# Kernel optimization log

Measured on AMD Instinct MI355X. Metric: run time of the kernel, lower is better.

The kernel has to match this reference:

```python
import jax, jax.numpy as jnp
import numpy as np

N = 100000
E = 1600000
F_IN = 512
H1, C1 = 8, 8          # conv1: 8 heads x 8 channels, concat -> 64
H2, C2 = 1, 16         # conv2: 1 head x num_classes=16, mean
NEG_SLOPE = 0.2


def setup_inputs() -> dict:
    key = jax.random.key(0)
    ks = jax.random.split(key, 10)
    x = jax.random.normal(ks[0], (N, F_IN), dtype=jnp.float32)
    edge_index = jax.random.randint(ks[1], (2, E), 0, N, dtype=jnp.int64)
    s1 = 1.0 / np.sqrt(F_IN)
    s2 = 1.0 / np.sqrt(H1 * C1)
    W1 = jax.random.normal(ks[2], (F_IN, H1 * C1), dtype=jnp.float32) * s1
    a1_src = jax.random.normal(ks[3], (H1, C1), dtype=jnp.float32) * 0.1
    a1_dst = jax.random.normal(ks[4], (H1, C1), dtype=jnp.float32) * 0.1
    b1 = jnp.zeros((H1 * C1,), dtype=jnp.float32)
    W2 = jax.random.normal(ks[5], (H1 * C1, H2 * C2), dtype=jnp.float32) * s2
    a2_src = jax.random.normal(ks[6], (H2, C2), dtype=jnp.float32) * 0.1
    a2_dst = jax.random.normal(ks[7], (H2, C2), dtype=jnp.float32) * 0.1
    b2 = jnp.zeros((C2,), dtype=jnp.float32)
    return {"x": x, "edge_index": edge_index, "W1": W1, "a1_src": a1_src,
            "a1_dst": a1_dst, "b1": b1, "W2": W2, "a2_src": a2_src,
            "a2_dst": a2_dst, "b2": b2}


def _add_self_loops(edge_index, n):
    loops = jnp.arange(n, dtype=edge_index.dtype)
    return jnp.concatenate([edge_index, jnp.stack([loops, loops])], axis=1)


def gat_conv(x, edge_index, W, a_src, a_dst, bias, concat):
    # x: [N, Fin]; W: [Fin, H*C]; a_*: [H, C]
    n = x.shape[0]
    H, C = a_src.shape
    h = (x @ W).reshape(n, H, C)                      # [N, H, C]
    al_src = jnp.einsum('nhc,hc->nh', h, a_src)       # [N, H]
    al_dst = jnp.einsum('nhc,hc->nh', h, a_dst)
    src, dst = edge_index[0], edge_index[1]
    e = al_src[src] + al_dst[dst]                     # [E, H]
    e = jnp.where(e > 0, e, NEG_SLOPE * e)            # LeakyReLU
    # segment softmax over destination nodes
    m = jax.ops.segment_max(e, dst, num_segments=n)   # [N, H]
    ex = jnp.exp(e - m[dst])
    s = jax.ops.segment_sum(ex, dst, num_segments=n)  # [N, H]
    alpha = ex / s[dst]                               # [E, H]
    msg = h[src] * alpha[:, :, None]                  # [E, H, C]
    out = jax.ops.segment_sum(msg, dst, num_segments=n)  # [N, H, C]
    if concat:
        out = out.reshape(n, H * C)
    else:
        out = out.mean(axis=1)
    return out + bias


def reference(x, edge_index, W1, a1_src, a1_dst, b1, W2, a2_src, a2_dst, b2):
    ei = _add_self_loops(edge_index, x.shape[0])
    h = gat_conv(x, ei, W1, a1_src, a1_dst, b1, concat=True)
    h = jax.nn.elu(h)
    h = gat_conv(h, ei, W2, a2_src, a2_dst, b2, concat=False)
    return jax.nn.log_softmax(h, axis=1)
```

## Files before the change

### kernel.cpp

```cpp
#include <hip/hip_runtime.h>
#include <math.h>

#define F_IN 512
#define NHEAD1 8
#define NC1 8
#define F1 64
#define NC2 16
#define NEG_SLOPE 0.2f
#define BSHIFT 7
#define PART_G 512
#define BUILD_CAP 4608

static __device__ __forceinline__ float leaky(float v) {
    return v > 0.0f ? v : NEG_SLOPE * v;
}

__global__ __launch_bounds__(256) void k_gemm1(const float* __restrict__ x,
                                               const float* __restrict__ W,
                                               float* __restrict__ h1, int N) {
    __shared__ float xs[64][33];
    __shared__ float wsm[32][64];
    const int tid = threadIdx.x;
    const int tx = tid & 15, ty = tid >> 4;
    const int row0 = blockIdx.x * 64;
    float acc[4][4] = {};

    for (int k0 = 0; k0 < F_IN; k0 += 32) {
        {
            int r = tid >> 3;
            int c = (tid & 7) * 4;
            #pragma unroll
            for (int rr = 0; rr < 64; rr += 32) {
                int gr = row0 + r + rr;
                float4 v = make_float4(0.f, 0.f, 0.f, 0.f);
                if (gr < N) v = *(const float4*)(x + (size_t)gr * F_IN + k0 + c);
                xs[r + rr][c + 0] = v.x; xs[r + rr][c + 1] = v.y;
                xs[r + rr][c + 2] = v.z; xs[r + rr][c + 3] = v.w;
            }
            int wr = tid >> 4;
            int wc = (tid & 15) * 4;
            #pragma unroll
            for (int rr = 0; rr < 32; rr += 16) {
                *(float4*)(&wsm[wr + rr][wc]) =
                    *(const float4*)(W + (size_t)(k0 + wr + rr) * F1 + wc);
            }
        }
        __syncthreads();
        #pragma unroll
        for (int k = 0; k < 32; ++k) {
            float a[4], b[4];
            #pragma unroll
            for (int i = 0; i < 4; ++i) a[i] = xs[ty * 4 + i][k];
            #pragma unroll
            for (int j = 0; j < 4; ++j) b[j] = wsm[k][tx * 4 + j];
            #pragma unroll
            for (int i = 0; i < 4; ++i)
                #pragma unroll
                for (int j = 0; j < 4; ++j) acc[i][j] += a[i] * b[j];
        }
        __syncthreads();
    }
    #pragma unroll
    for (int i = 0; i < 4; ++i) {
        int gr = row0 + ty * 4 + i;
        if (gr < N) {
            float4 v = make_float4(acc[i][0], acc[i][1], acc[i][2], acc[i][3]);
            *(float4*)(h1 + (size_t)gr * F1 + tx * 4) = v;
        }
    }
}

__global__ void k_prep1(const float* __restrict__ h1, const float* __restrict__ a1s,
                        const float* __restrict__ a1d, float* __restrict__ al1s,
                        float* __restrict__ al1d, int NH) {
    int t = blockIdx.x * blockDim.x + threadIdx.x;
    if (t >= NH) return;
    int h = t & 7;
    const float* hp = h1 + (size_t)t * NC1;
    float4 v0 = *(const float4*)hp;
    float4 v1 = *(const float4*)(hp + 4);
    const float* as = a1s + h * NC1;
    const float* ad = a1d + h * NC1;
    al1s[t] = v0.x * as[0] + v0.y * as[1] + v0.z * as[2] + v0.w * as[3]
            + v1.x * as[4] + v1.y * as[5] + v1.z * as[6] + v1.w * as[7];
    al1d[t] = v0.x * ad[0] + v0.y * ad[1] + v0.z * ad[2] + v0.w * ad[3]
            + v1.x * ad[4] + v1.y * ad[5] + v1.z * ad[6] + v1.w * ad[7];
}

__global__ __launch_bounds__(256) void k_bcount(const int* __restrict__ ei,
                                                int* __restrict__ counts,
                                                int E, int NBUCK, int chunk) {
    __shared__ int cnt[1024];
    const int g = blockIdx.x, tid = threadIdx.x;
    for (int i = tid; i < NBUCK; i += 256) cnt[i] = 0;
    __syncthreads();
    int lo = g * chunk, hi = lo + chunk;
    if (hi > E) hi = E;
    for (int e = lo + tid; e < hi; e += 256)
        atomicAdd(&cnt[ei[E + e] >> BSHIFT], 1);
    __syncthreads();
    for (int k = tid; k < NBUCK; k += 256)
        counts[k * PART_G + g] = cnt[k];
}

__global__ __launch_bounds__(256) void k_scan_block(const int* __restrict__ in,
                                                    int* __restrict__ out,
                                                    int* __restrict__ blocksum, int L) {
    __shared__ int sdata[256];
    int t = threadIdx.x;
    int i = blockIdx.x * 256 + t;
    int v = (i < L) ? in[i] : 0;
    sdata[t] = v;
    __syncthreads();
    for (int off = 1; off < 256; off <<= 1) {
        int add = (t >= off) ? sdata[t - off] : 0;
        __syncthreads();
        sdata[t] += add;
        __syncthreads();
    }
    if (i < L) out[i] = sdata[t] - v;
    if (t == 255) blocksum[blockIdx.x] = sdata[t];
}

__global__ void k_scan_carry(const int* __restrict__ blocksum,
                             int* __restrict__ blockoffset, int NB) {
    int lane = threadIdx.x;
    int carry = 0;
    for (int base = 0; base < NB; base += 64) {
        int i = base + lane;
        int v = (i < NB) ? blocksum[i] : 0;
        int x = v;
        #pragma unroll
        for (int off = 1; off < 64; off <<= 1) {
            int y = __shfl_up(x, off);
            if (lane >= off) x += y;
        }
        if (i < NB) blockoffset[i] = carry + x - v;
        carry += __shfl(x, 63);
    }
}

__global__ void k_scan_addg(int* __restrict__ out, const int* __restrict__ boff, int L) {
    int i = blockIdx.x * blockDim.x + threadIdx.x;
    if (i < L) out[i] += boff[i >> 8];
}

__global__ __launch_bounds__(256) void k_bscatter(const int* __restrict__ ei,
                                                  const int* __restrict__ offs,
                                                  unsigned long long* __restrict__ packed,
                                                  int E, int NBUCK, int chunk) {
    __shared__ int cur[1024];
    const int g = blockIdx.x, tid = threadIdx.x;
    for (int k = tid; k < NBUCK; k += 256) cur[k] = offs[k * PART_G + g];
    __syncthreads();
    int lo = g * chunk, hi = lo + chunk;
    if (hi > E) hi = E;
    for (int e = lo + tid; e < hi; e += 256) {
        int src = ei[e], dst = ei[E + e];
        int pos = atomicAdd(&cur[dst >> BSHIFT], 1);
        packed[pos] = ((unsigned long long)(unsigned)dst << 32) | (unsigned)src;
    }
}

__global__ __launch_bounds__(256) void k_bbuild(const unsigned long long* __restrict__ packed,
                                                const int* __restrict__ offs,
                                                int* __restrict__ rowptr,
                                                int* __restrict__ esrc,
                                                int E, int N, int NBUCK) {
    __shared__ int sdeg[128], sinc[128], scur[128];
    __shared__ int sbuf[BUILD_CAP];
    const int k = blockIdx.x, tid = threadIdx.x;
    const int s = offs[k * PART_G];
    const int e = (k + 1 < NBUCK) ? offs[(k + 1) * PART_G] : E;
    const int cnt = e - s;
    if (tid < 128) sdeg[tid] = 0;
    __syncthreads();
    for (int i = tid; i < cnt; i += 256) {
        int dl = ((int)(packed[s + i] >> 32)) & 127;
        atomicAdd(&sdeg[dl], 1);
    }
    __syncthreads();
    if (tid < 128) sinc[tid] = sdeg[tid];
    __syncthreads();
    for (int off = 1; off < 128; off <<= 1) {
        int add = (tid < 128 && tid >= off) ? sinc[tid - off] : 0;
        __syncthreads();
        if (tid < 128) sinc[tid] += add;
        __syncthreads();
    }
    int nd = N - (k << BSHIFT);
    if (nd > 128) nd = 128;
    if (tid < nd) {
        int excl = sinc[tid] - sdeg[tid];
        rowptr[(k << BSHIFT) + tid] = s + excl;
        scur[tid] = excl;
    }
    if (k == 0 && tid == 0) rowptr[N] = E;
    __syncthreads();
    if (cnt <= BUILD_CAP) {
        for (int i = tid; i < cnt; i += 256) {
            unsigned long long p = packed[s + i];
            int dl = ((int)(p >> 32)) & 127;
            int pos = atomicAdd(&scur[dl], 1);
            sbuf[pos] = (int)p;
        }
        __syncthreads();
        for (int i = tid; i < cnt; i += 256) esrc[s + i] = sbuf[i];
    } else {
        for (int i = tid; i < cnt; i += 256) {
            unsigned long long p = packed[s + i];
            int dl = ((int)(p >> 32)) & 127;
            int pos = atomicAdd(&scur[dl], 1);
            esrc[s + pos] = (int)p;
        }
    }
}

__global__ __launch_bounds__(256) void k_agg1(
    const float* __restrict__ h1, const float* __restrict__ al1s,
    const float* __restrict__ al1d, const int* __restrict__ rowptr,
    const int* __restrict__ esrc, const float* __restrict__ b1,
    const float* __restrict__ W2, const float* __restrict__ a2s,
    const float* __restrict__ a2d, float* __restrict__ h2,
    float* __restrict__ al2s, float* __restrict__ al2d, int N) {
    const int lane = threadIdx.x & 63;
    const int wv = threadIdx.x >> 6;
    const int n = blockIdx.x * 4 + wv;
    const int h = lane >> 3;
    const int q = lane >> 4, c = lane & 15;
    if (n >= N) return;

    float w2reg[16];
    #pragma unroll
    for (int j = 0; j < 16; ++j) w2reg[j] = W2[(q * 16 + j) * NC2 + c];
    const float b1l = b1[lane];
    const float a2sc = a2s[c], a2dc = a2d[c];

    const float aldh = al1d[n * 8 + h];
    float w0 = __expf(leaky(al1s[n * 8 + h] + aldh));
    float s = w0;
    float acc = w0 * h1[(size_t)n * F1 + lane];

    const int start = rowptr[n], end = rowptr[n + 1];
    for (int base = start; base < end; base += 64) {
        int cntv = end - base;
        if (cntv > 64) cntv = 64;
        int msrc = (lane < cntv) ? esrc[base + lane] : 0;
        for (int j = 0; j < cntv; ++j) {
            int src = __shfl(msrc, j);
            float w = __expf(leaky(al1s[src * 8 + h] + aldh));
            float hv = h1[(size_t)src * F1 + lane];
            s += w;
            acc = fmaf(w, hv, acc);
        }
    }
    float v = acc / s + b1l;
    v = v > 0.0f ? v : expm1f(v);
    float part = 0.f;
    #pragma unroll
    for (int j = 0; j < 16; ++j)
        part += __shfl(v, q * 16 + j) * w2reg[j];
    part += __shfl_xor(part, 16);
    part += __shfl_xor(part, 32);
    float ts = part * a2sc, td = part * a2dc;
    #pragma unroll
    for (int off = 1; off < 16; off <<= 1) {
        ts += __shfl_xor(ts, off);
        td += __shfl_xor(td, off);
    }
    if (lane < 16) h2[(size_t)n * NC2 + c] = part;
    if (lane == 0) { al2s[n] = ts; al2d[n] = td; }
}

__global__ __launch_bounds__(256) void k_agg2(
    const float* __restrict__ h2, const float* __restrict__ al2s,
    const float* __restrict__ al2d, const int* __restrict__ rowptr,
    const int* __restrict__ esrc, const float* __restrict__ b2,
    float* __restrict__ out, int N) {
    const int lane = threadIdx.x & 63;
    const int wv = threadIdx.x >> 6;
    const int n = blockIdx.x * 4 + wv;
    const int q = lane >> 4, c = lane & 15;
    if (n >= N) return;
    const float b2c = b2[c];
    const float ald = al2d[n];
    float s, acc;
    if (q == 0) {
        float w0 = __expf(leaky(al2s[n] + ald));
        s = w0;
        acc = w0 * h2[(size_t)n * NC2 + c];
    } else {
        s = 0.f; acc = 0.f;
    }
    const int start = rowptr[n], end = rowptr[n + 1];
    for (int k = start + q; k < end; k += 4) {
        int src = esrc[k];
        float w = __expf(leaky(al2s[src] + ald));
        float hv = h2[(size_t)src * NC2 + c];
        s += w;
        acc = fmaf(w, hv, acc);
    }
    s += __shfl_xor(s, 16);   acc += __shfl_xor(acc, 16);
    s += __shfl_xor(s, 32);   acc += __shfl_xor(acc, 32);
    float v = acc / s + b2c;
    float mm = v;
    #pragma unroll
    for (int off = 1; off < 16; off <<= 1) mm = fmaxf(mm, __shfl_xor(mm, off));
    float se = __expf(v - mm);
    #pragma unroll
    for (int off = 1; off < 16; off <<= 1) se += __shfl_xor(se, off);
    if (lane < 16) out[(size_t)n * NC2 + c] = v - (logf(se) + mm);
}

extern "C" void kernel_launch(void* const* d_in, const int* in_sizes, int n_in,
                              void* d_out, int out_size, void* d_ws, size_t ws_size,
                              hipStream_t stream) {
    const float* x      = (const float*)d_in[0];
    const int*   ei     = (const int*)d_in[1];
    const float* W1     = (const float*)d_in[2];
    const float* a1_src = (const float*)d_in[3];
    const float* a1_dst = (const float*)d_in[4];
    const float* b1     = (const float*)d_in[5];
    const float* W2     = (const float*)d_in[6];
    const float* a2_src = (const float*)d_in[7];
    const float* a2_dst = (const float*)d_in[8];
    const float* b2     = (const float*)d_in[9];
    float* out = (float*)d_out;

    const int N = in_sizes[0] / F_IN;
    const int E = in_sizes[1] / 2;
    const int NH = N * NHEAD1;
    const int NBUCK = (N + 127) >> BSHIFT;
    const int L = NBUCK * PART_G;
    const int NB = (L + 255) / 256;
    const int chunk = (E + PART_G - 1) / PART_G;

    char* base = (char*)d_ws;
    size_t off = 0;
    auto alloc = [&](size_t bytes, size_t align) -> void* {
        off = (off + align - 1) & ~(align - 1);
        void* p = base + off; off += bytes; return p;
    };
    float* h1   = (float*)alloc((size_t)N * F1 * 4, 16);
    float* al1s = (float*)alloc((size_t)NH * 4, 16);
    float* al1d = (float*)alloc((size_t)NH * 4, 16);
    float* h2   = (float*)alloc((size_t)N * NC2 * 4, 16);
    float* al2s = (float*)alloc((size_t)N * 4, 16);
    float* al2d = (float*)alloc((size_t)N * 4, 16);
    int* rowptr = (int*)alloc((size_t)(N + 1) * 4, 16);
    int* esrc   = (int*)alloc((size_t)E * 4, 16);
    char* tbase = (char*)h1;
    unsigned long long* packed = (unsigned long long*)tbase;
    int* counts   = (int*)(tbase + (size_t)E * 8);
    int* offs     = counts + L;
    int* blocksum = offs + L;
    int* boffset  = blocksum + NB;

    const int B = 256;
    auto blocks = [](long long cnt, int b) { return (int)((cnt + b - 1) / b); };

    k_bcount<<<PART_G, 256, 0, stream>>>(ei, counts, E, NBUCK, chunk);
    k_scan_block<<<NB, 256, 0, stream>>>(counts, offs, blocksum, L);
    k_scan_carry<<<1, 64, 0, stream>>>(blocksum, boffset, NB);
    k_scan_addg<<<blocks(L, B), B, 0, stream>>>(offs, boffset, L);
    k_bscatter<<<PART_G, 256, 0, stream>>>(ei, offs, packed, E, NBUCK, chunk);
    k_bbuild<<<NBUCK, 256, 0, stream>>>(packed, offs, rowptr, esrc, E, N, NBUCK);

    k_gemm1<<<dim3((N + 63) / 64), dim3(256), 0, stream>>>(x, W1, h1, N);
    k_prep1<<<blocks(NH, B), B, 0, stream>>>(h1, a1_src, a1_dst, al1s, al1d, NH);
    k_agg1<<<blocks(N, 4), 256, 0, stream>>>(h1, al1s, al1d, rowptr, esrc,
                                             b1, W2, a2_src, a2_dst,
                                             h2, al2s, al2d, N);
    k_agg2<<<blocks(N, 4), 256, 0, stream>>>(h2, al2s, al2d, rowptr, esrc, b2, out, N);
}
```

Baseline: 585.8 us.

## Fuse attention logits into GEMM epilogue, transpose x tile, pack edges into 32 bits

Computes the per-head source and destination attention logits in the GEMM1 epilogue with a lane-pair shuffle, which removes the separate k_prep1 kernel and its re-read of h1. The x tile is now stored transposed in shared memory, so the inner loop reads float4 vectors instead of scalar strided loads. Edge packing for the CSR build shrinks from 64-bit to 32-bit words (7-bit local destination plus a 20-bit source), halving scatter and build traffic. The 20-bit source field only holds node ids below about one million.

```diff
diff --git a/kernel.cpp b/kernel.cpp
--- a/kernel.cpp
+++ b/kernel.cpp
@@ -17,26 +17,33 @@
 
 __global__ __launch_bounds__(256) void k_gemm1(const float* __restrict__ x,
                                                const float* __restrict__ W,
-                                               float* __restrict__ h1, int N) {
-    __shared__ float xs[64][33];
+                                               const float* __restrict__ a1s,
+                                               const float* __restrict__ a1d,
+                                               float* __restrict__ h1,
+                                               float* __restrict__ al1s,
+                                               float* __restrict__ al1d, int N) {
+    __shared__ float xs[32][68];
     __shared__ float wsm[32][64];
     const int tid = threadIdx.x;
     const int tx = tid & 15, ty = tid >> 4;
     const int row0 = blockIdx.x * 64;
+    const int r = tid & 63;
+    const int kq = tid >> 6;
     float acc[4][4] = {};
 
     for (int k0 = 0; k0 < F_IN; k0 += 32) {
         {
-            int r = tid >> 3;
-            int c = (tid & 7) * 4;
-            #pragma unroll
-            for (int rr = 0; rr < 64; rr += 32) {
-                int gr = row0 + r + rr;
-                float4 v = make_float4(0.f, 0.f, 0.f, 0.f);
-                if (gr < N) v = *(const float4*)(x + (size_t)gr * F_IN + k0 + c);
-                xs[r + rr][c + 0] = v.x; xs[r + rr][c + 1] = v.y;
-                xs[r + rr][c + 2] = v.z; xs[r + rr][c + 3] = v.w;
+            int gr = row0 + r;
+            float4 v0 = make_float4(0.f, 0.f, 0.f, 0.f), v1 = v0;
+            if (gr < N) {
+                const float* p = x + (size_t)gr * F_IN + k0 + kq * 8;
+                v0 = *(const float4*)p;
+                v1 = *(const float4*)(p + 4);
             }
+            xs[kq * 8 + 0][r] = v0.x; xs[kq * 8 + 1][r] = v0.y;
+            xs[kq * 8 + 2][r] = v0.z; xs[kq * 8 + 3][r] = v0.w;
+            xs[kq * 8 + 4][r] = v1.x; xs[kq * 8 + 5][r] = v1.y;
+            xs[kq * 8 + 6][r] = v1.z; xs[kq * 8 + 7][r] = v1.w;
             int wr = tid >> 4;
             int wc = (tid & 15) * 4;
             #pragma unroll
@@ -48,43 +55,42 @@
         __syncthreads();
         #pragma unroll
         for (int k = 0; k < 32; ++k) {
-            float a[4], b[4];
-            #pragma unroll
-            for (int i = 0; i < 4; ++i) a[i] = xs[ty * 4 + i][k];
-            #pragma unroll
-            for (int j = 0; j < 4; ++j) b[j] = wsm[k][tx * 4 + j];
-            #pragma unroll
-            for (int i = 0; i < 4; ++i)
-                #pragma unroll
-                for (int j = 0; j < 4; ++j) acc[i][j] += a[i] * b[j];
-        }
-        __syncthreads();
-    }
+            float4 a = *(const float4*)(&xs[k][ty * 4]);
+            float4 b = *(const float4*)(&wsm[k][tx * 4]);
+            acc[0][0] = fmaf(a.x, b.x, acc[0][0]); acc[0][1] = fmaf(a.x, b.y, acc[0][1]);
+            acc[0][2] = fmaf(a.x, b.z, acc[0][2]); acc[0][3] = fmaf(a.x, b.w, acc[0][3]);
+            acc[1][0] = fmaf(a.y, b.x, acc[1][0]); acc[1][1] = fmaf(a.y, b.y, acc[1][1]);
+            acc[1][2] = fmaf(a.y, b.z, acc[1][2]); acc[1][3] = fmaf(a.y, b.w, acc[1][3]);
+            acc[2][0] = fmaf(a.z, b.x, acc[2][0]); acc[2][1] = fmaf(a.z, b.y, acc[2][1]);
+            acc[2][2] = fmaf(a.z, b.z, acc[2][2]); acc[2][3] = fmaf(a.z, b.w, acc[2][3]);
+            acc[3][0] = fmaf(a.w, b.x, acc[3][0]); acc[3][1] = fmaf(a.w, b.y, acc[3][1]);
+            acc[3][2] = fmaf(a.w, b.z, acc[3][2]); acc[3][3] = fmaf(a.w, b.w, acc[3][3]);
+        }
+        __syncthreads();
+    }
+    const int h = tx >> 1;
+    const float* as = a1s + h * 8 + (tx & 1) * 4;
+    const float* ad = a1d + h * 8 + (tx & 1) * 4;
+    float4 asv = *(const float4*)as;
+    float4 adv = *(const float4*)ad;
     #pragma unroll
     for (int i = 0; i < 4; ++i) {
         int gr = row0 + ty * 4 + i;
+        float ps = acc[i][0] * asv.x + acc[i][1] * asv.y
+                 + acc[i][2] * asv.z + acc[i][3] * asv.w;
+        float pd = acc[i][0] * adv.x + acc[i][1] * adv.y
+                 + acc[i][2] * adv.z + acc[i][3] * adv.w;
+        ps += __shfl_xor(ps, 1);
+        pd += __shfl_xor(pd, 1);
         if (gr < N) {
-            float4 v = make_float4(acc[i][0], acc[i][1], acc[i][2], acc[i][3]);
-            *(float4*)(h1 + (size_t)gr * F1 + tx * 4) = v;
-        }
-    }
-}
-
-__global__ void k_prep1(const float* __restrict__ h1, const float* __restrict__ a1s,
-                        const float* __restrict__ a1d, float* __restrict__ al1s,
-                        float* __restrict__ al1d, int NH) {
-    int t = blockIdx.x * blockDim.x + threadIdx.x;
-    if (t >= NH) return;
-    int h = t & 7;
-    const float* hp = h1 + (size_t)t * NC1;
-    float4 v0 = *(const float4*)hp;
-    float4 v1 = *(const float4*)(hp + 4);
-    const float* as = a1s + h * NC1;
-    const float* ad = a1d + h * NC1;
-    al1s[t] = v0.x * as[0] + v0.y * as[1] + v0.z * as[2] + v0.w * as[3]
-            + v1.x * as[4] + v1.y * as[5] + v1.z * as[6] + v1.w * as[7];
-    al1d[t] = v0.x * ad[0] + v0.y * ad[1] + v0.z * ad[2] + v0.w * ad[3]
-            + v1.x * ad[4] + v1.y * ad[5] + v1.z * ad[6] + v1.w * ad[7];
+            *(float4*)(h1 + (size_t)gr * F1 + tx * 4) =
+                make_float4(acc[i][0], acc[i][1], acc[i][2], acc[i][3]);
+            if ((tx & 1) == 0) {
+                al1s[gr * 8 + h] = ps;
+                al1d[gr * 8 + h] = pd;
+            }
+        }
+    }
 }
 
 __global__ __launch_bounds__(256) void k_bcount(const int* __restrict__ ei,
@@ -147,7 +153,7 @@
 
 __global__ __launch_bounds__(256) void k_bscatter(const int* __restrict__ ei,
                                                   const int* __restrict__ offs,
-                                                  unsigned long long* __restrict__ packed,
+                                                  unsigned* __restrict__ packed,
                                                   int E, int NBUCK, int chunk) {
     __shared__ int cur[1024];
     const int g = blockIdx.x, tid = threadIdx.x;
@@ -158,11 +164,11 @@
     for (int e = lo + tid; e < hi; e += 256) {
         int src = ei[e], dst = ei[E + e];
         int pos = atomicAdd(&cur[dst >> BSHIFT], 1);
-        packed[pos] = ((unsigned long long)(unsigned)dst << 32) | (unsigned)src;
-    }
-}
-
-__global__ __launch_bounds__(256) void k_bbuild(const unsigned long long* __restrict__ packed,
+        packed[pos] = ((unsigned)(dst & 127) << 20) | (unsigned)src;
+    }
+}
+
+__global__ __launch_bounds__(256) void k_bbuild(const unsigned* __restrict__ packed,
                                                 const int* __restrict__ offs,
                                                 int* __restrict__ rowptr,
                                                 int* __restrict__ esrc,
@@ -175,10 +181,8 @@
     const int cnt = e - s;
     if (tid < 128) sdeg[tid] = 0;
     __syncthreads();
-    for (int i = tid; i < cnt; i += 256) {
-        int dl = ((int)(packed[s + i] >> 32)) & 127;
-        atomicAdd(&sdeg[dl], 1);
-    }
+    for (int i = tid; i < cnt; i += 256)
+        atomicAdd(&sdeg[packed[s + i] >> 20], 1);
     __syncthreads();
     if (tid < 128) sinc[tid] = sdeg[tid];
     __syncthreads();
@@ -199,19 +203,17 @@
     __syncthreads();
     if (cnt <= BUILD_CAP) {
         for (int i = tid; i < cnt; i += 256) {
-            unsigned long long p = packed[s + i];
-            int dl = ((int)(p >> 32)) & 127;
-            int pos = atomicAdd(&scur[dl], 1);
-            sbuf[pos] = (int)p;
+            unsigned p = packed[s + i];
+            int pos = atomicAdd(&scur[p >> 20], 1);
+            sbuf[pos] = (int)(p & 0xFFFFFu);
         }
         __syncthreads();
         for (int i = tid; i < cnt; i += 256) esrc[s + i] = sbuf[i];
     } else {
         for (int i = tid; i < cnt; i += 256) {
-            unsigned long long p = packed[s + i];
-            int dl = ((int)(p >> 32)) & 127;
-            int pos = atomicAdd(&scur[dl], 1);
-            esrc[s + pos] = (int)p;
+            unsigned p = packed[s + i];
+            int pos = atomicAdd(&scur[p >> 20], 1);
+            esrc[s + pos] = (int)(p & 0xFFFFFu);
         }
     }
 }
@@ -350,8 +352,8 @@
     int* rowptr = (int*)alloc((size_t)(N + 1) * 4, 16);
     int* esrc   = (int*)alloc((size_t)E * 4, 16);
     char* tbase = (char*)h1;
-    unsigned long long* packed = (unsigned long long*)tbase;
-    int* counts   = (int*)(tbase + (size_t)E * 8);
+    unsigned* packed = (unsigned*)tbase;
+    int* counts   = (int*)(tbase + (size_t)E * 4);
     int* offs     = counts + L;
     int* blocksum = offs + L;
     int* boffset  = blocksum + NB;
@@ -366,8 +368,8 @@
     k_bscatter<<<PART_G, 256, 0, stream>>>(ei, offs, packed, E, NBUCK, chunk);
     k_bbuild<<<NBUCK, 256, 0, stream>>>(packed, offs, rowptr, esrc, E, N, NBUCK);
 
-    k_gemm1<<<dim3((N + 63) / 64), dim3(256), 0, stream>>>(x, W1, h1, N);
-    k_prep1<<<blocks(NH, B), B, 0, stream>>>(h1, a1_src, a1_dst, al1s, al1d, NH);
+    k_gemm1<<<dim3((N + 63) / 64), dim3(256), 0, stream>>>(x, W1, a1_src, a1_dst,
+                                                           h1, al1s, al1d, N);
     k_agg1<<<blocks(N, 4), 256, 0, stream>>>(h1, al1s, al1d, rowptr, esrc,
                                              b1, W2, a2_src, a2_dst,
                                              h2, al2s, al2d, N);
```

Measured after the change: 586.8 us. Within noise of the previous version (+0.2%).
